# Kernel tuning notes

Measured on AMD Instinct MI355X. Metric: run time of the kernel, lower is better.

The kernel has to match this reference:

```python
import jax, jax.numpy as jnp
import numpy as np

DG = 8   # deformable groups
K = 3    # DCNv2 kernel size


def conv1x1(x, w):
    return jnp.einsum('bhwc,cf->bhwf', x, w)


def conv3x3_same(x, w, b):
    out = jax.lax.conv_general_dilated(x, w, (1, 1), 'SAME',
                                       dimension_numbers=('NHWC', 'HWIO', 'NHWC'))
    return out + b


def dcn_v2(x, offset, mask, weight, bias):
    # x: [B,H,W,C]; offset: [B,H,W,DG,K*K,2] (dy,dx); mask: [B,H,W,DG,K*K]
    B, H, W, C = x.shape
    cpg = C // DG
    ky, kx = jnp.meshgrid(jnp.arange(K) - (K // 2), jnp.arange(K) - (K // 2), indexing='ij')
    ky = ky.reshape(-1).astype(x.dtype)  # [K*K]
    kx = kx.reshape(-1).astype(x.dtype)
    iy = jnp.arange(H, dtype=x.dtype)[None, :, None, None, None]
    ix = jnp.arange(W, dtype=x.dtype)[None, None, :, None, None]
    yp = iy + ky + offset[..., 0]   # [B,H,W,DG,KK] sample rows
    xp = ix + kx + offset[..., 1]   # sample cols

    # group-major flattened feature map for gather: [B,DG,H*W,cpg]
    xt = jnp.transpose(x.reshape(B, H, W, DG, cpg), (0, 3, 1, 2, 4)).reshape(B, DG, H * W, cpg)

    def gather(yi, xi):
        valid = ((yi >= 0) & (yi < H) & (xi >= 0) & (xi < W)).astype(x.dtype)
        yc = jnp.clip(yi, 0, H - 1)
        xc = jnp.clip(xi, 0, W - 1)
        flat = (yc * W + xc).astype(jnp.int32)               # [B,H,W,DG,KK]
        idx = jnp.transpose(flat, (0, 3, 1, 2, 4)).reshape(B, DG, -1)
        v = jnp.take_along_axis(xt, idx[..., None], axis=2)  # [B,DG,H*W*KK,cpg]
        v = v.reshape(B, DG, H, W, K * K, cpg)
        v = jnp.transpose(v, (0, 2, 3, 1, 4, 5))             # [B,H,W,DG,KK,cpg]
        return v * valid[..., None]

    y0 = jnp.floor(yp); x0 = jnp.floor(xp)
    wy = (yp - y0)[..., None]; wx = (xp - x0)[..., None]
    val = (gather(y0, x0) * (1 - wy) * (1 - wx)
           + gather(y0, x0 + 1) * (1 - wy) * wx
           + gather(y0 + 1, x0) * wy * (1 - wx)
           + gather(y0 + 1, x0 + 1) * wy * wx)
    val = val * mask[..., None]                               # modulated sampling
    # [B,H,W,DG,KK,cpg] -> [B,H,W,KK,C] (global channel = g*cpg + r)
    val = jnp.transpose(val, (0, 1, 2, 4, 3, 5)).reshape(B, H, W, K * K, C)
    out = jnp.einsum('bhwkc,kcf->bhwf', val, weight.reshape(K * K, C, -1))
    return out + bias


def setup_inputs() -> dict:
    key = jax.random.key(0)
    ks = jax.random.split(key, 8)
    B, H, W, Cf, Cc, F = 4, 64, 64, 256, 256, 256
    fine = jax.random.normal(ks[0], (B, H, W, Cf), jnp.float32)
    coarse = jax.random.normal(ks[1], (B, H // 2, W // 2, Cc), jnp.float32)
    attend_w = jax.random.normal(ks[2], (Cf, Cf), jnp.float32) * 0.05
    select_w = jax.random.normal(ks[3], (Cf, F), jnp.float32) * 0.05
    offset_w = jax.random.normal(ks[4], (F + Cc, 2 * F), jnp.float32) * 0.05
    om_w = jax.random.normal(ks[5], (3, 3, 2 * F, DG * 3 * K * K), jnp.float32) * 0.01
    om_b = jnp.zeros((DG * 3 * K * K,), jnp.float32)
    dcn_w = jax.random.normal(ks[6], (3, 3, Cc, F), jnp.float32) * 0.05
    dcn_b = jnp.zeros((F,), jnp.float32)
    return {'fine': fine, 'coarse': coarse, 'attend_w': attend_w, 'select_w': select_w,
            'offset_w': offset_w, 'om_w': om_w, 'om_b': om_b, 'dcn_w': dcn_w, 'dcn_b': dcn_b}


def reference(fine, coarse, attend_w, select_w, offset_w, om_w, om_b, dcn_w, dcn_b):
    B, H, W, Cf = fine.shape
    Cc = coarse.shape[-1]
    # BilinearInterpolation: upsample coarse to fine resolution
    coarse_up = jax.image.resize(coarse, (B, H, W, Cc), 'bilinear')
    # FeatureSelection: GAP -> 1x1 sigmoid attention, residual gate, 1x1 proj
    attn = jax.nn.sigmoid(conv1x1(jnp.mean(fine, axis=(1, 2), keepdims=True), attend_w))
    fine_cal = conv1x1(fine * (attn + 1.0), select_w)
    # offset features from concat(selected fine, 2*coarse)
    align = conv1x1(jnp.concatenate([fine_cal, coarse_up * 2.0], axis=-1), offset_w)
    # DCNv2 internal offset/mask conv (3x3) on alignment features
    om = conv3x3_same(align, om_w, om_b)          # [B,H,W,DG*3*K*K]
    n_off = DG * 2 * K * K
    off = om[..., :n_off].reshape(B, H, W, DG, K * K, 2)
    mask = jax.nn.sigmoid(om[..., n_off:]).reshape(B, H, W, DG, K * K)
    aligned = dcn_v2(coarse_up, off, mask, dcn_w, dcn_b)
    return jax.nn.relu(aligned) + fine_cal
```

## Files before the change

kernel.cpp:

```cpp
#include <hip/hip_runtime.h>
#include <math.h>


typedef __attribute__((ext_vector_type(8))) short bf16x8;
typedef __attribute__((ext_vector_type(4))) short bf16x4;
typedef __attribute__((ext_vector_type(4))) float f32x4;
#define MFMA16(a,b,c) __builtin_amdgcn_mfma_f32_16x16x32_bf16(a,b,c,0,0,0)

__device__ inline short f2b(float x){
  union { float f; unsigned u; } v; v.f = x;
  unsigned r = v.u + 0x7FFFu + ((v.u >> 16) & 1u);
  return (short)(r >> 16);
}
__device__ inline float b2f(short s){
  union { unsigned u; float f; } v;
  v.u = ((unsigned)(unsigned short)s) << 16;
  return v.f;
}

#define OFS_GATE  1024u
#define OFS_PART  2048u
#define OFS_CUPB  264192u
#define OFS_FCAL  4458496u
#define OFS_ALGB  8652800u
#define OFS_OM    12847104u
#define OFS_DWB   16386048u
#define OFS_OMWB  16680960u
#define OFS_SWB   17270784u
#define OFS_OWB   17401856u

__global__ __launch_bounds__(256) void k_gap(const float* __restrict__ fine,
                                             float* __restrict__ part){
  __shared__ float red[4*256];
  int b = blockIdx.x >> 6, chunk = blockIdx.x & 63;
  int c4 = threadIdx.x & 63, rl = threadIdx.x >> 6;
  const float4* F4 = (const float4*)fine;
  float4 s = {0.f,0.f,0.f,0.f};
  for (int it = 0; it < 16; ++it){
    int row = chunk*64 + it*4 + rl;
    float4 v = F4[((size_t)(b*4096 + row))*64 + c4];
    s.x += v.x; s.y += v.y; s.z += v.z; s.w += v.w;
  }
  *(float4*)&red[rl*256 + c4*4] = s;
  __syncthreads();
  int c = threadIdx.x;
  part[(size_t)blockIdx.x*256 + c] = red[c] + red[256+c] + red[512+c] + red[768+c];
}

__global__ __launch_bounds__(256) void k_misc(const float* __restrict__ part,
                                              const float* __restrict__ aw,
                                              float* __restrict__ gate,
                                              const float* __restrict__ dw,
                                              const float* __restrict__ omw,
                                              const float* __restrict__ ow,
                                              const float* __restrict__ sw,
                                              short* __restrict__ dwb,
                                              short* __restrict__ omwb,
                                              short* __restrict__ owb,
                                              short* __restrict__ swb,
                                              const float* __restrict__ coarse,
                                              short* __restrict__ cupb){
  int blk = blockIdx.x;
  if (blk < 4){
    __shared__ float m[256];
    int b = blk, f = threadIdx.x;
    float sm = 0.f;
    for (int ch = 0; ch < 64; ++ch) sm += part[(size_t)(b*64 + ch)*256 + f];
    m[f] = sm * (1.f/4096.f);
    __syncthreads();
    float s = 0.f;
    for (int c = 0; c < 256; ++c) s += m[c] * aw[c*256 + f];
    gate[b*256 + f] = 1.f + 1.f/(1.f + expf(-s));
  } else if (blk < 292){
    int t = (blk - 4)*256 + threadIdx.x;
    int l = t & 63, nt = (t >> 6) & 15, ksg = t >> 10;
    int n = nt*16 + (l & 15);
    int kb = ksg*32 + (l >> 4)*8;
    bf16x8 o;
#pragma unroll
    for (int j = 0; j < 8; ++j) o[j] = f2b(dw[(size_t)(kb + j)*256 + n]);
    ((bf16x8*)dwb)[t] = o;
  } else if (blk < 868){
    int t = (blk - 292)*256 + threadIdx.x;
    int l = t & 63, nt = (t >> 6) & 15, ksg = t >> 10;
    int n = nt*16 + (l & 15);
    int kb = ksg*32 + (l >> 4)*8;
    bf16x8 o;
#pragma unroll
    for (int j = 0; j < 8; ++j)
      o[j] = (n < 216) ? f2b(omw[(size_t)(kb + j)*216 + n]) : (short)0;
    ((bf16x8*)omwb)[t] = o;
  } else if (blk < 996){
    int t = (blk - 868)*256 + threadIdx.x;
    int l = t & 63, nt = (t >> 6) & 31, ksg = t >> 11;
    int n = nt*16 + (l & 15);
    int kb = ksg*32 + (l >> 4)*8;
    float sc = (kb >= 256) ? 2.f : 1.f;
    bf16x8 o;
#pragma unroll
    for (int j = 0; j < 8; ++j) o[j] = f2b(sc * ow[(size_t)(kb + j)*512 + n]);
    ((bf16x8*)owb)[t] = o;
  } else if (blk < 1124){
    int t = (blk - 996)*256 + threadIdx.x;
    int l = t & 63, nt = (t >> 6) & 15, ksg = t >> 10;
    int n = nt*16 + (l & 15);
    int kb = ksg*32 + (l >> 4)*8;
    bf16x8 o;
#pragma unroll
    for (int j = 0; j < 8; ++j) o[j] = f2b(sw[(size_t)(kb + j)*256 + n]);
    ((bf16x8*)swb)[t] = o;
  } else {
    int idx = (blk - 1124)*256 + threadIdx.x;
    int c4 = idx & 63, x = (idx >> 6) & 63, y = (idx >> 12) & 63, b = idx >> 18;
    float fy = 0.5f*y - 0.25f, fx = 0.5f*x - 0.25f;
    float yf = floorf(fy), xf = floorf(fx);
    float wy = fy - yf, wx = fx - xf;
    int r0 = max(0, min(31, (int)yf)), r1 = max(0, min(31, (int)yf + 1));
    int c0 = max(0, min(31, (int)xf)), c1 = max(0, min(31, (int)xf + 1));
    const float4* src = (const float4*)coarse;
    float4 v00 = src[((b*32 + r0)*32 + c0)*64 + c4];
    float4 v01 = src[((b*32 + r0)*32 + c1)*64 + c4];
    float4 v10 = src[((b*32 + r1)*32 + c0)*64 + c4];
    float4 v11 = src[((b*32 + r1)*32 + c1)*64 + c4];
    float w00 = (1.f-wy)*(1.f-wx), w01 = (1.f-wy)*wx, w10 = wy*(1.f-wx), w11 = wy*wx;
    bf16x4 o = { f2b(v00.x*w00 + v01.x*w01 + v10.x*w10 + v11.x*w11),
                 f2b(v00.y*w00 + v01.y*w01 + v10.y*w10 + v11.y*w11),
                 f2b(v00.z*w00 + v01.z*w01 + v10.z*w10 + v11.z*w11),
                 f2b(v00.w*w00 + v01.w*w01 + v10.w*w10 + v11.w*w11) };
    ((bf16x4*)cupb)[idx] = o;
  }
}

#define FST 264
__global__ __launch_bounds__(512) void k_fa(const float* __restrict__ fine,
                                            const float* __restrict__ gate,
                                            const short* __restrict__ swb,
                                            const short* __restrict__ owb,
                                            const short* __restrict__ cupb,
                                            float* __restrict__ fcal,
                                            short* __restrict__ algb){
  __shared__ float g4[256];
  __shared__ short ab[32*FST];
  int bid = ((blockIdx.x & 7) << 6) | (blockIdx.x >> 3);
  int m0 = bid*32, b = m0 >> 12;
  int tid = threadIdx.x, lane = tid & 63, wave = tid >> 6;
  int arow = lane & 15, aquad = lane >> 4;
  if (tid < 256) g4[tid] = gate[b*256 + tid];
  __syncthreads();
  const float4* F4 = (const float4*)(fine + (size_t)m0*256);
  const float4* G4 = (const float4*)g4;
  for (int it = 0; it < 4; ++it){
    int idx = it*512 + tid;
    int row = idx >> 6, c4 = idx & 63;
    float4 v = F4[row*64 + c4];
    float4 gg = G4[c4];
    bf16x4 s4 = { f2b(v.x*gg.x), f2b(v.y*gg.y), f2b(v.z*gg.z), f2b(v.w*gg.w) };
    *(bf16x4*)&ab[row*FST + c4*4] = s4;
  }
  __syncthreads();
  f32x4 acc[2][2];
#pragma unroll
  for (int s = 0; s < 2; ++s)
#pragma unroll
    for (int t = 0; t < 2; ++t) acc[s][t] = (f32x4){0.f,0.f,0.f,0.f};
  const bf16x8* W8 = (const bf16x8*)swb;
  for (int ks = 0; ks < 8; ++ks){
    bf16x8 a0 = *(const bf16x8*)&ab[arow*FST + ks*32 + aquad*8];
    bf16x8 a1 = *(const bf16x8*)&ab[(16 + arow)*FST + ks*32 + aquad*8];
    const bf16x8* wp = W8 + ((size_t)(ks*16 + wave*2))*64 + lane;
#pragma unroll
    for (int t = 0; t < 2; ++t){
      bf16x8 bw = wp[t*64];
      acc[0][t] = MFMA16(a0, bw, acc[0][t]);
      acc[1][t] = MFMA16(a1, bw, acc[1][t]);
    }
  }
  __syncthreads();
#pragma unroll
  for (int t = 0; t < 2; ++t){
    int f = wave*32 + t*16 + arow;
#pragma unroll
    for (int s = 0; s < 2; ++s)
#pragma unroll
      for (int r = 0; r < 4; ++r){
        int mloc = s*16 + aquad*4 + r;
        float v = acc[s][t][r];
        fcal[(size_t)(m0 + mloc)*256 + f] = v;
        ab[mloc*FST + f] = f2b(v);
      }
  }
  __syncthreads();
  f32x4 acc2[2][4];
#pragma unroll
  for (int s = 0; s < 2; ++s)
#pragma unroll
    for (int t = 0; t < 4; ++t) acc2[s][t] = (f32x4){0.f,0.f,0.f,0.f};
  const bf16x8* OW8 = (const bf16x8*)owb;
  for (int ks = 0; ks < 16; ++ks){
    bf16x8 a0, a1;
    if (ks < 8){
      a0 = *(const bf16x8*)&ab[arow*FST + ks*32 + aquad*8];
      a1 = *(const bf16x8*)&ab[(16 + arow)*FST + ks*32 + aquad*8];
    } else {
      int ko = (ks - 8)*32 + aquad*8;
      a0 = *(const bf16x8*)(cupb + (size_t)(m0 + arow)*256 + ko);
      a1 = *(const bf16x8*)(cupb + (size_t)(m0 + 16 + arow)*256 + ko);
    }
    const bf16x8* wp = OW8 + ((size_t)(ks*32 + wave*4))*64 + lane;
#pragma unroll
    for (int t = 0; t < 4; ++t){
      bf16x8 bw = wp[t*64];
      acc2[0][t] = MFMA16(a0, bw, acc2[0][t]);
      acc2[1][t] = MFMA16(a1, bw, acc2[1][t]);
    }
  }
#pragma unroll
  for (int t = 0; t < 4; ++t){
    int n = wave*64 + t*16 + arow;
#pragma unroll
    for (int s = 0; s < 2; ++s)
#pragma unroll
      for (int r = 0; r < 4; ++r){
        int m = m0 + s*16 + aquad*4 + r;
        algb[(size_t)m*512 + n] = f2b(acc2[s][t][r]);
      }
  }
}

#define XSW 256
__global__ __launch_bounds__(512) void k_om(const short* __restrict__ algb,
                                            const short* __restrict__ omwb,
                                            const float* __restrict__ omb,
                                            float* __restrict__ om){
  __shared__ short xbuf[66*XSW];
  int blk = ((blockIdx.x & 7) << 5) | (blockIdx.x >> 3);
  int m0 = blk*64;
  int b = m0 >> 12, y = (m0 >> 6) & 63;
  int tid = threadIdx.x;
  int lane = tid & 63, wave = tid >> 6;
  int arow = lane & 15, aquad = lane >> 4;
  f32x4 acc[4][2];
#pragma unroll
  for (int mi = 0; mi < 4; ++mi)
#pragma unroll
    for (int t = 0; t < 2; ++t) acc[mi][t] = (f32x4){0.f,0.f,0.f,0.f};
  const bf16x8* W8 = (const bf16x8*)omwb;
  for (int ky = 0; ky < 3; ++ky){
    int yy = y + ky - 1;
    if ((unsigned)yy >= 64u) continue;
    const short* srow = algb + (size_t)((b*64 + yy)*64)*512;
    for (int h = 0; h < 2; ++h){
      __syncthreads();
      for (int it = 0; it < 5; ++it){
        int u = it*512 + tid;
        if (u < 2112){
          int xx = u >> 5, cu = u & 31;
          int gx = xx - 1;
          bf16x8 v = (bf16x8){0,0,0,0,0,0,0,0};
          if ((unsigned)gx < 64u)
            v = *(const bf16x8*)(srow + (size_t)gx*512 + h*256 + cu*8);
          *(bf16x8*)&xbuf[xx*XSW + ((cu*8) ^ ((xx & 7) << 3))] = v;
        }
      }
      __syncthreads();
#pragma unroll
      for (int kx = 0; kx < 3; ++kx){
        for (int s = 0; s < 8; ++s){
          int ksg = ky*48 + kx*16 + h*8 + s;
          bf16x8 a[4];
#pragma unroll
          for (int mi = 0; mi < 4; ++mi){
            int row = mi*16 + arow + kx;
            a[mi] = *(const bf16x8*)&xbuf[row*XSW + ((s*32 + aquad*8) ^ ((row & 7) << 3))];
          }
          const bf16x8* wp = W8 + ((size_t)(ksg*16 + wave*2))*64 + lane;
#pragma unroll
          for (int t = 0; t < 2; ++t){
            bf16x8 bw = wp[t*64];
#pragma unroll
            for (int mi = 0; mi < 4; ++mi)
              acc[mi][t] = MFMA16(a[mi], bw, acc[mi][t]);
          }
        }
      }
    }
  }
#pragma unroll
  for (int t = 0; t < 2; ++t){
    int f = wave*32 + t*16 + arow;
    if (f < 216){
      float bias = omb[f];
      bool is_mask = (f >= 144);
#pragma unroll
      for (int mi = 0; mi < 4; ++mi)
#pragma unroll
        for (int r = 0; r < 4; ++r){
          int m = m0 + mi*16 + aquad*4 + r;
          float v = acc[mi][t][r] + bias;
          if (is_mask) v = 1.f/(1.f + expf(-v));
          om[(size_t)m*216 + f] = v;
        }
    }
  }
}

#define VST 776
__global__ __launch_bounds__(512) void k_dcn(const short* __restrict__ cupb,
                                             const float* __restrict__ om,
                                             const short* __restrict__ dwb,
                                             const float* __restrict__ db,
                                             const float* __restrict__ fcal,
                                             float* __restrict__ out){
  __shared__ short valb[32*VST];
  int bid = ((blockIdx.x & 7) << 6) | (blockIdx.x >> 3);
  int m0 = bid*32;
  int b = m0 >> 12, y = (m0 & 4095) >> 6, x0 = m0 & 63;
  int tid = threadIdx.x;
  int lane = tid & 63, wave = tid >> 6;
  int unit = tid >> 2, lane4 = tid & 3;
  int arow = lane & 15, aquad = lane >> 4;
  f32x4 acc[2][2];
#pragma unroll
  for (int s = 0; s < 2; ++s)
#pragma unroll
    for (int t = 0; t < 2; ++t) acc[s][t] = (f32x4){0.f,0.f,0.f,0.f};
  const short* cpb = cupb + (size_t)b*4096*256;
  const bf16x8* W8 = (const bf16x8*)dwb;

  for (int ph = 0; ph < 3; ++ph){
    __syncthreads();
    for (int it = 0; it < 6; ++it){
      int u = it*128 + unit;
      int i = u / 24; int r = u - i*24; int g = r / 3; int kk = r - g*3;
      const float* omp = om + (size_t)(m0 + i)*216;
      int k = ph*3 + kk;
      float dy = omp[(g*9 + k)*2 + 0];
      float dx = omp[(g*9 + k)*2 + 1];
      float mv = omp[144 + g*9 + k];
      float yp = (float)(y + ph - 1) + dy;
      float xp = (float)(x0 + i + kk - 1) + dx;
      float yf = floorf(yp), xf = floorf(xp);
      float wy = yp - yf, wx = xp - xf;
      int iy = (int)yf, ix = (int)xf;
      float wA = (1.f-wy)*(1.f-wx), wB = (1.f-wy)*wx, wC = wy*(1.f-wx), wD = wy*wx;
      bool y0ok = (unsigned)iy < 64u, y1ok = (unsigned)(iy+1) < 64u;
      bool x0ok = (unsigned)ix < 64u, x1ok = (unsigned)(ix+1) < 64u;
      if (!(y0ok && x0ok)) wA = 0.f;
      if (!(y0ok && x1ok)) wB = 0.f;
      if (!(y1ok && x0ok)) wC = 0.f;
      if (!(y1ok && x1ok)) wD = 0.f;
      int y0c = min(max(iy, 0), 63), y1c = min(max(iy + 1, 0), 63);
      int x0c = min(max(ix, 0), 63), x1c = min(max(ix + 1, 0), 63);
      int cofs = g*32 + lane4*8;
      bf16x8 l00 = *(const bf16x8*)(cpb + (size_t)(y0c*64 + x0c)*256 + cofs);
      bf16x8 l01 = *(const bf16x8*)(cpb + (size_t)(y0c*64 + x1c)*256 + cofs);
      bf16x8 l10 = *(const bf16x8*)(cpb + (size_t)(y1c*64 + x0c)*256 + cofs);
      bf16x8 l11 = *(const bf16x8*)(cpb + (size_t)(y1c*64 + x1c)*256 + cofs);
      bf16x8 o;
#pragma unroll
      for (int j = 0; j < 8; ++j){
        float v = wA*b2f(l00[j]) + wB*b2f(l01[j]) + wC*b2f(l10[j]) + wD*b2f(l11[j]);
        o[j] = f2b(v * mv);
      }
      *(bf16x8*)&valb[i*VST + kk*256 + g*32 + lane4*8] = o;
    }
    __syncthreads();
    const bf16x8* wb = W8 + ((size_t)((ph*24)*16 + wave*2))*64 + lane;
    bf16x8 c0 = wb[0], c1 = wb[64];
    for (int ks = 0; ks < 24; ++ks){
      bf16x8 a0 = *(const bf16x8*)&valb[arow*VST + ks*32 + aquad*8];
      bf16x8 a1 = *(const bf16x8*)&valb[(16 + arow)*VST + ks*32 + aquad*8];
      bf16x8 n0, n1;
      if (ks < 23){ n0 = wb[(ks+1)*1024]; n1 = wb[(ks+1)*1024 + 64]; }
      acc[0][0] = MFMA16(a0, c0, acc[0][0]);
      acc[1][0] = MFMA16(a1, c0, acc[1][0]);
      acc[0][1] = MFMA16(a0, c1, acc[0][1]);
      acc[1][1] = MFMA16(a1, c1, acc[1][1]);
      if (ks < 23){ c0 = n0; c1 = n1; }
    }
  }
#pragma unroll
  for (int t = 0; t < 2; ++t){
    int f = wave*32 + t*16 + (lane & 15);
    float bias = db[f];
#pragma unroll
    for (int s = 0; s < 2; ++s)
#pragma unroll
      for (int r = 0; r < 4; ++r){
        int m = m0 + s*16 + aquad*4 + r;
        out[(size_t)m*256 + f] = fmaxf(acc[s][t][r] + bias, 0.f) + fcal[(size_t)m*256 + f];
      }
  }
}

extern "C" void kernel_launch(void* const* d_in, const int* in_sizes, int n_in,
                              void* d_out, int out_size, void* d_ws, size_t ws_size,
                              hipStream_t stream){
  const float* fine     = (const float*)d_in[0];
  const float* coarse   = (const float*)d_in[1];
  const float* attend_w = (const float*)d_in[2];
  const float* select_w = (const float*)d_in[3];
  const float* offset_w = (const float*)d_in[4];
  const float* om_w     = (const float*)d_in[5];
  const float* om_b     = (const float*)d_in[6];
  const float* dcn_w    = (const float*)d_in[7];
  const float* dcn_b    = (const float*)d_in[8];
  float* out = (float*)d_out;
  float* ws  = (float*)d_ws;

  float* gate = ws + OFS_GATE;
  float* part = ws + OFS_PART;
  short* cupb = (short*)(ws + OFS_CUPB);
  float* fcal = ws + OFS_FCAL;
  short* algb = (short*)(ws + OFS_ALGB);
  float* om   = ws + OFS_OM;
  short* dwb  = (short*)(ws + OFS_DWB);
  short* omwb = (short*)(ws + OFS_OMWB);
  short* swb  = (short*)(ws + OFS_SWB);
  short* owb  = (short*)(ws + OFS_OWB);

  hipLaunchKernelGGL(k_gap,  dim3(256),  dim3(256), 0, stream, fine, part);
  hipLaunchKernelGGL(k_misc, dim3(5220), dim3(256), 0, stream, part, attend_w, gate,
                     dcn_w, om_w, offset_w, select_w, dwb, omwb, owb, swb, coarse, cupb);
  hipLaunchKernelGGL(k_fa,   dim3(512),  dim3(512), 0, stream, fine, gate, swb, owb,
                     cupb, fcal, algb);
  hipLaunchKernelGGL(k_om,   dim3(256),  dim3(512), 0, stream, algb, omwb, om_b, om);
  hipLaunchKernelGGL(k_dcn,  dim3(512),  dim3(512), 0, stream, cupb, om, dwb, dcn_b, fcal, out);
  (void)in_sizes; (void)n_in; (void)out_size; (void)ws_size;
}
```

Baseline: 223.3 us.

## Double-buffer the 3x3 offset-conv LDS tile and prefetch the next phase into registers

The k_om kernel now splits its six input-row phases over two shared-memory buffers. Global loads for the next phase are issued into registers before the MFMA work on the current phase and written to the other buffer afterwards, which halves the barriers per phase and hides load latency behind compute. The XOR swizzle is replaced with a padded row stride, and the kx/s loops are fully unrolled. In exchange it uses about twice the LDS and more registers, and it always loads zero rows at the image border instead of skipping them.

```diff
diff --git a/kernel.cpp b/kernel.cpp
--- a/kernel.cpp
+++ b/kernel.cpp
@@ -227,12 +227,12 @@
   }
 }
 
-#define XSW 256
-__global__ __launch_bounds__(512) void k_om(const short* __restrict__ algb,
-                                            const short* __restrict__ omwb,
-                                            const float* __restrict__ omb,
-                                            float* __restrict__ om){
-  __shared__ short xbuf[66*XSW];
+#define XST2 264
+__global__ __launch_bounds__(512, 2) void k_om(const short* __restrict__ algb,
+                                               const short* __restrict__ omwb,
+                                               const float* __restrict__ omb,
+                                               float* __restrict__ om){
+  __shared__ short xbuf[2][66*XST2];
   int blk = ((blockIdx.x & 7) << 5) | (blockIdx.x >> 3);
   int m0 = blk*64;
   int b = m0 >> 12, y = (m0 >> 6) & 63;
@@ -245,46 +245,76 @@
 #pragma unroll
     for (int t = 0; t < 2; ++t) acc[mi][t] = (f32x4){0.f,0.f,0.f,0.f};
   const bf16x8* W8 = (const bf16x8*)omwb;
-  for (int ky = 0; ky < 3; ++ky){
-    int yy = y + ky - 1;
-    if ((unsigned)yy >= 64u) continue;
-    const short* srow = algb + (size_t)((b*64 + yy)*64)*512;
-    for (int h = 0; h < 2; ++h){
-      __syncthreads();
+  const size_t rowbase = (size_t)(b*64)*64*512;
+
+  int su[5], sxx[5], scu[5];
+#pragma unroll
+  for (int it = 0; it < 5; ++it){
+    int u = it*512 + tid;
+    su[it] = (u < 2112);
+    sxx[it] = u >> 5;
+    scu[it] = u & 31;
+  }
+
+  bf16x8 stg[5];
+  {
+    int yy = y - 1; bool yok = (unsigned)yy < 64u;
+#pragma unroll
+    for (int it = 0; it < 5; ++it){
+      stg[it] = (bf16x8){0,0,0,0,0,0,0,0};
+      int gx = sxx[it] - 1;
+      if (su[it] && yok && (unsigned)gx < 64u)
+        stg[it] = *(const bf16x8*)(algb + rowbase + ((size_t)yy*64 + gx)*512 + scu[it]*8);
+    }
+#pragma unroll
+    for (int it = 0; it < 5; ++it)
+      if (su[it]) *(bf16x8*)&xbuf[0][sxx[it]*XST2 + scu[it]*8] = stg[it];
+  }
+  __syncthreads();
+
+  for (int ph = 0; ph < 6; ++ph){
+    bf16x8 nst[5];
+    if (ph < 5){
+      int np = ph + 1;
+      int yy = y + (np >> 1) - 1; int h = np & 1;
+      bool yok = (unsigned)yy < 64u;
+#pragma unroll
       for (int it = 0; it < 5; ++it){
-        int u = it*512 + tid;
-        if (u < 2112){
-          int xx = u >> 5, cu = u & 31;
-          int gx = xx - 1;
-          bf16x8 v = (bf16x8){0,0,0,0,0,0,0,0};
-          if ((unsigned)gx < 64u)
-            v = *(const bf16x8*)(srow + (size_t)gx*512 + h*256 + cu*8);
-          *(bf16x8*)&xbuf[xx*XSW + ((cu*8) ^ ((xx & 7) << 3))] = v;
+        nst[it] = (bf16x8){0,0,0,0,0,0,0,0};
+        int gx = sxx[it] - 1;
+        if (su[it] && yok && (unsigned)gx < 64u)
+          nst[it] = *(const bf16x8*)(algb + rowbase + ((size_t)yy*64 + gx)*512 + h*256 + scu[it]*8);
+      }
+    }
+    const short* xb = xbuf[ph & 1];
+    int kybase = (ph >> 1)*48 + (ph & 1)*8;
+#pragma unroll
+    for (int kx = 0; kx < 3; ++kx){
+#pragma unroll
+      for (int s = 0; s < 8; ++s){
+        int ksg = kybase + kx*16 + s;
+        bf16x8 a[4];
+#pragma unroll
+        for (int mi = 0; mi < 4; ++mi)
+          a[mi] = *(const bf16x8*)&xb[(mi*16 + arow + kx)*XST2 + s*32 + aquad*8];
+        const bf16x8* wp = W8 + ((size_t)(ksg*16 + wave*2))*64 + lane;
+#pragma unroll
+        for (int t = 0; t < 2; ++t){
+          bf16x8 bw = wp[t*64];
+#pragma unroll
+          for (int mi = 0; mi < 4; ++mi)
+            acc[mi][t] = MFMA16(a[mi], bw, acc[mi][t]);
         }
       }
-      __syncthreads();
-#pragma unroll
-      for (int kx = 0; kx < 3; ++kx){
-        for (int s = 0; s < 8; ++s){
-          int ksg = ky*48 + kx*16 + h*8 + s;
-          bf16x8 a[4];
-#pragma unroll
-          for (int mi = 0; mi < 4; ++mi){
-            int row = mi*16 + arow + kx;
-            a[mi] = *(const bf16x8*)&xbuf[row*XSW + ((s*32 + aquad*8) ^ ((row & 7) << 3))];
-          }
-          const bf16x8* wp = W8 + ((size_t)(ksg*16 + wave*2))*64 + lane;
-#pragma unroll
-          for (int t = 0; t < 2; ++t){
-            bf16x8 bw = wp[t*64];
-#pragma unroll
-            for (int mi = 0; mi < 4; ++mi)
-              acc[mi][t] = MFMA16(a[mi], bw, acc[mi][t]);
-          }
-        }
-      }
-    }
-  }
+    }
+    if (ph < 5){
+#pragma unroll
+      for (int it = 0; it < 5; ++it)
+        if (su[it]) *(bf16x8*)&xbuf[(ph + 1) & 1][sxx[it]*XST2 + scu[it]*8] = nst[it];
+    }
+    __syncthreads();
+  }
+
 #pragma unroll
   for (int t = 0; t < 2; ++t){
     int f = wave*32 + t*16 + arow;
```

Measured after the change: 223.6 us. No clear change (+0.1%).
